# Kernel optimization log

Measured on AMD Instinct MI355X. Metric: run time of the kernel, lower is better.

## Reference

```python
import jax, jax.numpy as jnp
import numpy as np

LN_EPS = 1e-5
DEG_EPS = 1e-6
H = 256
N_VAR = 100000
NUM_CON = 50000
E = 300000


def setup_inputs() -> dict:
    key = jax.random.key(0)
    ks = jax.random.split(key, 8)
    s = 1.0 / np.sqrt(H)
    s2 = 1.0 / np.sqrt(H + 1)
    return {
        "x_var": jax.random.normal(ks[0], (N_VAR, H), dtype=jnp.float32),
        "src": jax.random.randint(ks[1], (E,), 0, N_VAR, dtype=jnp.int32),
        "dst": jax.random.randint(ks[2], (E,), 0, NUM_CON, dtype=jnp.int32),
        "clue_values": jax.random.normal(ks[3], (NUM_CON,), dtype=jnp.float32),
        "num_con": NUM_CON,
        "msg_W": jax.random.uniform(ks[4], (H, H), jnp.float32, -s, s),
        "msg_b": jax.random.uniform(ks[5], (H,), jnp.float32, -s, s),
        "update_W": jax.random.uniform(ks[6], (H, H + 1), jnp.float32, -s2, s2),
        "update_b": jax.random.uniform(ks[7], (H,), jnp.float32, -s2, s2),
        "ln_w": jnp.ones((H,), jnp.float32),
        "ln_b": jnp.zeros((H,), jnp.float32),
    }


def reference(x_var, src, dst, clue_values, num_con, msg_W, msg_b, update_W, update_b, ln_w, ln_b):
    # gather + linear message transform: (E, H)
    msgs = x_var[src] @ msg_W.T + msg_b
    # degree-normalized scatter-add into constraints: (num_con, H)
    agg = jax.ops.segment_sum(msgs, dst, num_segments=num_con)
    deg = jax.ops.segment_sum(jnp.ones((dst.shape[0],), msgs.dtype), dst, num_segments=num_con)
    agg = agg / (deg[:, None] + DEG_EPS)
    # concat clue scalar, update MLP, ReLU
    h = jnp.concatenate([agg, clue_values[:, None]], axis=1)
    out = jax.nn.relu(h @ update_W.T + update_b)
    # LayerNorm over last dim
    mu = out.mean(axis=-1, keepdims=True)
    var = out.var(axis=-1, keepdims=True)
    return (out - mu) * jax.lax.rsqrt(var + LN_EPS) * ln_w + ln_b
```

## Files before the change

### kernel.cpp

```cpp
#include <hip/hip_runtime.h>

#define HD 256
#define LN_EPS 1e-5f
#define DEG_EPS 1e-6f
#define CAP 64

typedef __attribute__((ext_vector_type(8))) short short8;
typedef __attribute__((ext_vector_type(4))) short s16x4;
typedef __attribute__((ext_vector_type(4))) float f32x4;
typedef __attribute__((ext_vector_type(4))) int i32x4;

__device__ inline unsigned short f2bf(float f) {
    union { float f; unsigned int u; } v; v.f = f;
    unsigned int r = v.u + 0x7FFFu + ((v.u >> 16) & 1u);
    return (unsigned short)(r >> 16);
}
__device__ inline float bf2f(unsigned short h) {
    union { unsigned int u; float f; } v; v.u = ((unsigned int)h) << 16;
    return v.f;
}
__device__ inline short8 cvt8(float4 u0, float4 u1) {
    short8 o;
    o[0] = (short)f2bf(u0.x); o[1] = (short)f2bf(u0.y);
    o[2] = (short)f2bf(u0.z); o[3] = (short)f2bf(u0.w);
    o[4] = (short)f2bf(u1.x); o[5] = (short)f2bf(u1.y);
    o[6] = (short)f2bf(u1.z); o[7] = (short)f2bf(u1.w);
    return o;
}

__global__ __launch_bounds__(256) void prep0_kernel(
    int* __restrict__ counts, int num_con,
    const float* __restrict__ msg_W, const float* __restrict__ msg_b,
    const float* __restrict__ upd_W,
    unsigned short* __restrict__ w12b, float* __restrict__ bv,
    float* __restrict__ ucol, int zb) {
    int b = blockIdx.x, tid = threadIdx.x;
    if (b < zb) {
        int i = (b * 256 + tid) * 4;
        if (i + 4 <= num_con) *(i32x4*)(counts + i) = (i32x4){0, 0, 0, 0};
        else for (; i < num_con; ++i) counts[i] = 0;
    } else {
        int j = b - zb, k = tid;
        float a0 = 0.f, a1 = 0.f, a2 = 0.f, a3 = 0.f, accb = 0.f;
#pragma unroll 2
        for (int m = 0; m < 256; m += 4) {
            float w0 = upd_W[j * 257 + m + 0];
            float w1 = upd_W[j * 257 + m + 1];
            float w2 = upd_W[j * 257 + m + 2];
            float w3 = upd_W[j * 257 + m + 3];
            a0 = fmaf(w0, msg_W[(m + 0) * 256 + k], a0);
            a1 = fmaf(w1, msg_W[(m + 1) * 256 + k], a1);
            a2 = fmaf(w2, msg_W[(m + 2) * 256 + k], a2);
            a3 = fmaf(w3, msg_W[(m + 3) * 256 + k], a3);
            accb = fmaf(w0, msg_b[m + 0], accb);
            accb = fmaf(w1, msg_b[m + 1], accb);
            accb = fmaf(w2, msg_b[m + 2], accb);
            accb = fmaf(w3, msg_b[m + 3], accb);
        }
        w12b[j * 256 + k] = f2bf((a0 + a1) + (a2 + a3));
        if (k == 0) { bv[j] = accb; ucol[j] = upd_W[j * 257 + 256]; }
    }
}

__global__ __launch_bounds__(256) void fill_kernel(
    const int* __restrict__ src, const int* __restrict__ dst,
    int* __restrict__ counts, int* __restrict__ eidx, int E) {
    int e = blockIdx.x * 256 + threadIdx.x;
    if (e >= E) return;
    int d = dst[e];
    int p = atomicAdd(&counts[d], 1);
    if (p < CAP) eidx[d * CAP + p] = src[e];
}

__global__ __launch_bounds__(256) void ygemm_kernel(
    const float* __restrict__ x, const unsigned short* __restrict__ w12b,
    unsigned short* __restrict__ y, int n_var, int ntiles) {

    __shared__ unsigned short sA[2][16 * 256];
    const int tid = threadIdx.x, w = tid >> 6, lane = tid & 63;
    const int lr = lane & 15, lg = lane >> 4;

    short8 bfr[4][8];
#pragma unroll
    for (int jt = 0; jt < 4; ++jt)
#pragma unroll
        for (int ks = 0; ks < 8; ++ks)
            bfr[jt][ks] = *(const short8*)(w12b + (w * 64 + jt * 16 + lr) * HD + lg * 8 + ks * 32);

    const int srow = tid >> 4, scol = (tid & 15) * 16;
    const int b0 = (srow * 512 + scol * 2) ^ ((srow & 7) << 4);
    const int b1 = (srow * 512 + scol * 2 + 16) ^ ((srow & 7) << 4);

    int rt = blockIdx.x;
    float4 u0, u1, u2, u3;
    if (rt < ntiles) {
        int arc = min(rt * 16 + srow, n_var - 1);
        const float* gp = x + (long)arc * HD + scol;
        u0 = *(const float4*)(gp);
        u1 = *(const float4*)(gp + 4);
        u2 = *(const float4*)(gp + 8);
        u3 = *(const float4*)(gp + 12);
    }

    int buf = 0;
#pragma unroll 1
    for (; rt < ntiles; ) {
        int r0 = rt * 16;
        *(short8*)((char*)&sA[buf][0] + b0) = cvt8(u0, u1);
        *(short8*)((char*)&sA[buf][0] + b1) = cvt8(u2, u3);

        __syncthreads();

        int nrt = rt + gridDim.x;
        {
            int prt = min(nrt, ntiles - 1);
            int arc = min(prt * 16 + srow, n_var - 1);
            const float* gp = x + (long)arc * HD + scol;
            u0 = *(const float4*)(gp);
            u1 = *(const float4*)(gp + 4);
            u2 = *(const float4*)(gp + 8);
            u3 = *(const float4*)(gp + 12);
        }

        short8 af[8];
#pragma unroll
        for (int ks = 0; ks < 8; ++ks) {
            int byte = (lr * 512 + (ks * 32 + lg * 8) * 2) ^ ((lr & 7) << 4);
            af[ks] = *(const short8*)((char*)&sA[buf][0] + byte);
        }

        f32x4 acc[4] = {{0.f,0.f,0.f,0.f},{0.f,0.f,0.f,0.f},{0.f,0.f,0.f,0.f},{0.f,0.f,0.f,0.f}};
#pragma unroll
        for (int ks = 0; ks < 8; ++ks)
#pragma unroll
            for (int jt = 0; jt < 4; ++jt)
                acc[jt] = __builtin_amdgcn_mfma_f32_16x16x32_bf16(af[ks], bfr[jt][ks], acc[jt], 0, 0, 0);

#pragma unroll
        for (int q = 0; q < 4; ++q) {
            int grow = r0 + lg * 4 + q;
            if (grow < n_var) {
                s16x4 o;
#pragma unroll
                for (int jt = 0; jt < 4; ++jt) o[jt] = (short)f2bf(acc[jt][q]);
                *(s16x4*)(y + (long)grow * HD + w * 64 + lr * 4) = o;
            }
        }
        buf ^= 1;
        rt = nrt;
    }
}

__global__ __launch_bounds__(256) void gatherln_kernel(
    const unsigned short* __restrict__ y, const int* __restrict__ counts,
    const int* __restrict__ eidx, const float* __restrict__ clue,
    const float* __restrict__ bv, const float* __restrict__ ucol,
    const float* __restrict__ upd_b,
    const float* __restrict__ ln_w, const float* __restrict__ ln_b,
    float* __restrict__ out, int num_con) {
    int row  = blockIdx.x * 4 + (threadIdx.x >> 6);
    int lane = threadIdx.x & 63;
    if (row >= num_con) return;
    int cnt = counts[row];
    int cgo = min(cnt, CAP);
    int sid = (lane < cgo) ? eidx[row * CAP + lane] : 0;
    float a0 = 0.f, a1 = 0.f, a2 = 0.f, a3 = 0.f;
#pragma unroll 1
    for (int i = 0; i < cgo; i += 8) {
        int s[8];
#pragma unroll
        for (int u = 0; u < 8; ++u) s[u] = __shfl(sid, i + u, 64);
        s16x4 v[8];
#pragma unroll
        for (int u = 0; u < 8; ++u)
            v[u] = *(const s16x4*)(y + (long)s[u] * HD + lane * 4);
#pragma unroll
        for (int u = 0; u < 8; ++u) {
            float wg = (i + u < cgo) ? 1.f : 0.f;
            a0 = fmaf(bf2f((unsigned short)v[u][0]), wg, a0);
            a1 = fmaf(bf2f((unsigned short)v[u][1]), wg, a1);
            a2 = fmaf(bf2f((unsigned short)v[u][2]), wg, a2);
            a3 = fmaf(bf2f((unsigned short)v[u][3]), wg, a3);
        }
    }
    int c0 = ((lane >> 4) << 6) + (lane & 15);
    float sc = 1.0f / ((float)cnt + DEG_EPS);
    float tc = (float)cnt * sc;
    float cl = clue[row];
    float z[4] = {a0, a1, a2, a3};
    float s = 0.f, s2 = 0.f;
#pragma unroll
    for (int jt = 0; jt < 4; ++jt) {
        int c = c0 + jt * 16;
        float zz = fmaxf(z[jt] * sc + tc * bv[c] + cl * ucol[c] + upd_b[c], 0.0f);
        z[jt] = zz;
        s += zz; s2 += zz * zz;
    }
#pragma unroll
    for (int m = 1; m < 64; m <<= 1) {
        s  += __shfl_xor(s,  m, 64);
        s2 += __shfl_xor(s2, m, 64);
    }
    float mu = s * (1.0f / HD);
    float var = s2 * (1.0f / HD) - mu * mu;
    float rs = rsqrtf(var + LN_EPS);
    float* gp = out + (long)row * HD;
#pragma unroll
    for (int jt = 0; jt < 4; ++jt) {
        int c = c0 + jt * 16;
        gp[c] = (z[jt] - mu) * rs * ln_w[c] + ln_b[c];
    }
}

extern "C" void kernel_launch(void* const* d_in, const int* in_sizes, int n_in,
                              void* d_out, int out_size, void* d_ws, size_t ws_size,
                              hipStream_t stream) {
    const float* x_var = (const float*)d_in[0];
    const int*   src   = (const int*)d_in[1];
    const int*   dst   = (const int*)d_in[2];
    const float* clue  = (const float*)d_in[3];
    const float* msg_W = (const float*)d_in[5];
    const float* msg_b = (const float*)d_in[6];
    const float* upd_W = (const float*)d_in[7];
    const float* upd_b = (const float*)d_in[8];
    const float* ln_w  = (const float*)d_in[9];
    const float* ln_b  = (const float*)d_in[10];

    int E = in_sizes[1];
    long n_x = in_sizes[0];
    int n_var = (int)(n_x / HD);
    int num_con = out_size / HD;
    int ntiles_v = (n_var + 15) / 16;

    char* ws = (char*)d_ws;
    int* counts = (int*)ws;
    int* eidx   = (int*)(ws + (((size_t)num_con * 4 + 255) & ~(size_t)255));
    char* after = (char*)(eidx + (size_t)num_con * CAP);
    size_t yoff = ((size_t)(after - ws) + 255) & ~(size_t)255;
    unsigned short* yv = (unsigned short*)(ws + yoff);
    size_t woff = (yoff + (size_t)n_var * HD * 2 + 255) & ~(size_t)255;
    unsigned short* w12b = (unsigned short*)(ws + woff);
    float* bvp  = (float*)(w12b + 256 * 256);
    float* ucol = bvp + 256;

    int zb = (num_con + 1023) / 1024;
    prep0_kernel<<<zb + 256, 256, 0, stream>>>(
        counts, num_con, msg_W, msg_b, upd_W, w12b, bvp, ucol, zb);

    fill_kernel<<<(E + 255) / 256, 256, 0, stream>>>(src, dst, counts, eidx, E);

    ygemm_kernel<<<1024, 256, 0, stream>>>(x_var, w12b, yv, n_var, ntiles_v);

    gatherln_kernel<<<(num_con + 3) / 4, 256, 0, stream>>>(
        yv, counts, eidx, clue, bvp, ucol, upd_b, ln_w, ln_b,
        (float*)d_out, num_con);
}
```

Before: 103.6 us.

## Split ygemm across 8 waves with 32 output columns each, remap gather layout

The y-GEMM kernel now runs 512 threads per block, with 8 waves each owning 32 output columns instead of 4 waves owning 64. This halves the per-wave B-fragment registers and accumulators, and each thread stages 8 floats instead of 16. Each row's y storage layout changes to packed pairs, so the gather/LayerNorm kernel remaps its column indices to match. The aim is more waves in flight to hide memory latency, at the cost of smaller 4-byte stores and more complex index math in the consumer.

```diff
diff --git a/kernel.cpp b/kernel.cpp
--- a/kernel.cpp
+++ b/kernel.cpp
@@ -19,12 +19,12 @@
     union { unsigned int u; float f; } v; v.u = ((unsigned int)h) << 16;
     return v.f;
 }
-__device__ inline short8 cvt8(float4 u0, float4 u1) {
+__device__ inline short8 cvt8(f32x4 u0, f32x4 u1) {
     short8 o;
-    o[0] = (short)f2bf(u0.x); o[1] = (short)f2bf(u0.y);
-    o[2] = (short)f2bf(u0.z); o[3] = (short)f2bf(u0.w);
-    o[4] = (short)f2bf(u1.x); o[5] = (short)f2bf(u1.y);
-    o[6] = (short)f2bf(u1.z); o[7] = (short)f2bf(u1.w);
+    o[0] = (short)f2bf(u0[0]); o[1] = (short)f2bf(u0[1]);
+    o[2] = (short)f2bf(u0[2]); o[3] = (short)f2bf(u0[3]);
+    o[4] = (short)f2bf(u1[0]); o[5] = (short)f2bf(u1[1]);
+    o[6] = (short)f2bf(u1[2]); o[7] = (short)f2bf(u1[3]);
     return o;
 }
 
@@ -72,7 +72,7 @@
     if (p < CAP) eidx[d * CAP + p] = src[e];
 }
 
-__global__ __launch_bounds__(256) void ygemm_kernel(
+__global__ __launch_bounds__(512) void ygemm_kernel(
     const float* __restrict__ x, const unsigned short* __restrict__ w12b,
     unsigned short* __restrict__ y, int n_var, int ntiles) {
 
@@ -80,34 +80,30 @@
     const int tid = threadIdx.x, w = tid >> 6, lane = tid & 63;
     const int lr = lane & 15, lg = lane >> 4;
 
-    short8 bfr[4][8];
-#pragma unroll
-    for (int jt = 0; jt < 4; ++jt)
+    short8 bfr[2][8];
+#pragma unroll
+    for (int jt = 0; jt < 2; ++jt)
 #pragma unroll
         for (int ks = 0; ks < 8; ++ks)
-            bfr[jt][ks] = *(const short8*)(w12b + (w * 64 + jt * 16 + lr) * HD + lg * 8 + ks * 32);
-
-    const int srow = tid >> 4, scol = (tid & 15) * 16;
-    const int b0 = (srow * 512 + scol * 2) ^ ((srow & 7) << 4);
-    const int b1 = (srow * 512 + scol * 2 + 16) ^ ((srow & 7) << 4);
+            bfr[jt][ks] = *(const short8*)(w12b + (w * 32 + jt * 16 + lr) * HD + lg * 8 + ks * 32);
+
+    const int srow = tid >> 5, scol = (tid & 31) * 8;
+    const int sb = (srow * 512 + scol * 2) ^ ((srow & 7) << 4);
 
     int rt = blockIdx.x;
-    float4 u0, u1, u2, u3;
+    f32x4 u0, u1;
     if (rt < ntiles) {
         int arc = min(rt * 16 + srow, n_var - 1);
-        const float* gp = x + (long)arc * HD + scol;
-        u0 = *(const float4*)(gp);
-        u1 = *(const float4*)(gp + 4);
-        u2 = *(const float4*)(gp + 8);
-        u3 = *(const float4*)(gp + 12);
+        const f32x4* gp = (const f32x4*)(x + (long)arc * HD + scol);
+        u0 = gp[0];
+        u1 = gp[1];
     }
 
     int buf = 0;
 #pragma unroll 1
     for (; rt < ntiles; ) {
         int r0 = rt * 16;
-        *(short8*)((char*)&sA[buf][0] + b0) = cvt8(u0, u1);
-        *(short8*)((char*)&sA[buf][0] + b1) = cvt8(u2, u3);
+        *(short8*)((char*)&sA[buf][0] + sb) = cvt8(u0, u1);
 
         __syncthreads();
 
@@ -115,11 +111,9 @@
         {
             int prt = min(nrt, ntiles - 1);
             int arc = min(prt * 16 + srow, n_var - 1);
-            const float* gp = x + (long)arc * HD + scol;
-            u0 = *(const float4*)(gp);
-            u1 = *(const float4*)(gp + 4);
-            u2 = *(const float4*)(gp + 8);
-            u3 = *(const float4*)(gp + 12);
+            const f32x4* gp = (const f32x4*)(x + (long)arc * HD + scol);
+            u0 = gp[0];
+            u1 = gp[1];
         }
 
         short8 af[8];
@@ -129,21 +123,20 @@
             af[ks] = *(const short8*)((char*)&sA[buf][0] + byte);
         }
 
-        f32x4 acc[4] = {{0.f,0.f,0.f,0.f},{0.f,0.f,0.f,0.f},{0.f,0.f,0.f,0.f},{0.f,0.f,0.f,0.f}};
+        f32x4 acc[2] = {{0.f,0.f,0.f,0.f},{0.f,0.f,0.f,0.f}};
 #pragma unroll
         for (int ks = 0; ks < 8; ++ks)
 #pragma unroll
-            for (int jt = 0; jt < 4; ++jt)
+            for (int jt = 0; jt < 2; ++jt)
                 acc[jt] = __builtin_amdgcn_mfma_f32_16x16x32_bf16(af[ks], bfr[jt][ks], acc[jt], 0, 0, 0);
 
 #pragma unroll
         for (int q = 0; q < 4; ++q) {
             int grow = r0 + lg * 4 + q;
             if (grow < n_var) {
-                s16x4 o;
-#pragma unroll
-                for (int jt = 0; jt < 4; ++jt) o[jt] = (short)f2bf(acc[jt][q]);
-                *(s16x4*)(y + (long)grow * HD + w * 64 + lr * 4) = o;
+                unsigned int pk = (unsigned int)f2bf(acc[0][q]) |
+                                  (((unsigned int)f2bf(acc[1][q])) << 16);
+                *(unsigned int*)(y + (long)grow * HD + w * 32 + lr * 2) = pk;
             }
         }
         buf ^= 1;
@@ -183,17 +176,19 @@
             a3 = fmaf(bf2f((unsigned short)v[u][3]), wg, a3);
         }
     }
-    int c0 = ((lane >> 4) << 6) + (lane & 15);
     float sc = 1.0f / ((float)cnt + DEG_EPS);
     float tc = (float)cnt * sc;
     float cl = clue[row];
     float z[4] = {a0, a1, a2, a3};
+    int tcol[4];
     float s = 0.f, s2 = 0.f;
 #pragma unroll
-    for (int jt = 0; jt < 4; ++jt) {
-        int c = c0 + jt * 16;
-        float zz = fmaxf(z[jt] * sc + tc * bv[c] + cl * ucol[c] + upd_b[c], 0.0f);
-        z[jt] = zz;
+    for (int c = 0; c < 4; ++c) {
+        int cc = lane * 4 + c;
+        int t = (cc & ~31) | ((cc & 1) << 4) | ((cc & 31) >> 1);
+        tcol[c] = t;
+        float zz = fmaxf(z[c] * sc + tc * bv[t] + cl * ucol[t] + upd_b[t], 0.0f);
+        z[c] = zz;
         s += zz; s2 += zz * zz;
     }
 #pragma unroll
@@ -206,9 +201,9 @@
     float rs = rsqrtf(var + LN_EPS);
     float* gp = out + (long)row * HD;
 #pragma unroll
-    for (int jt = 0; jt < 4; ++jt) {
-        int c = c0 + jt * 16;
-        gp[c] = (z[jt] - mu) * rs * ln_w[c] + ln_b[c];
+    for (int c = 0; c < 4; ++c) {
+        int t = tcol[c];
+        gp[t] = (z[c] - mu) * rs * ln_w[t] + ln_b[t];
     }
 }
 
@@ -249,7 +244,7 @@
 
     fill_kernel<<<(E + 255) / 256, 256, 0, stream>>>(src, dst, counts, eidx, E);
 
-    ygemm_kernel<<<1024, 256, 0, stream>>>(x_var, w12b, yv, n_var, ntiles_v);
+    ygemm_kernel<<<1024, 512, 0, stream>>>(x_var, w12b, yv, n_var, ntiles_v);
 
     gatherln_kernel<<<(num_con + 3) / 4, 256, 0, stream>>>(
         yv, counts, eidx, clue, bvp, ucol, upd_b, ln_w, ln_b,
```

After: 105.7 us. +2.1%, slower.
